# Kernel optimization log

Measured on AMD Instinct MI355X. Metric: run time of the kernel, lower is better.

The kernel has to match this reference:

```python
import jax, jax.numpy as jnp
import numpy as np

B, T, H, C = 32, 2048, 1024, 1024

def setup_inputs() -> dict:
    key = jax.random.key(0)
    k1, k2, k3, k4, k5, k6 = jax.random.split(key, 6)
    decoder_output = jax.random.normal(k1, (B, 1, H), dtype=jnp.float32)
    encoder_outputs = jax.random.normal(k2, (B, T, H), dtype=jnp.float32)
    scale = 1.0 / np.sqrt(H)
    W = jax.random.normal(k3, (H, C), dtype=jnp.float32) * scale
    V = jax.random.normal(k4, (H, C), dtype=jnp.float32) * scale
    b = jax.random.uniform(k5, (C,), dtype=jnp.float32, minval=-0.1, maxval=0.1)
    w = jax.random.normal(k6, (C, 1), dtype=jnp.float32) * (1.0 / np.sqrt(C))
    return {"decoder_output": decoder_output, "encoder_outputs": encoder_outputs,
            "W": W, "V": V, "b": b, "w": w}

def reference(decoder_output, encoder_outputs, W, V, b, w):
    # Additive (Bahdanau) content attention.
    dec_proj = jnp.einsum('bqh,hc->bqc', decoder_output, W)   # [B,1,C]
    enc_proj = jnp.einsum('bth,hc->btc', encoder_outputs, V)  # [B,T,C]
    energy = jnp.tanh(dec_proj + enc_proj + b)                # [B,T,C]
    scores = jnp.einsum('btc,c->bt', energy, w[:, 0])         # [B,T]
    alignment = jax.nn.softmax(scores, axis=-1)               # [B,T]
    context = jnp.einsum('bt,bth->bh', alignment, encoder_outputs)  # [B,H]
    return context
```

## Files before the change

### kernel.cpp

```cpp
#include <hip/hip_runtime.h>
#include <hip/hip_bf16.h>
#include <stdint.h>

#define Bn 32
#define Tn 2048
#define Hn 1024
#define Cn 1024

typedef short short8 __attribute__((ext_vector_type(8)));
typedef float floatx4 __attribute__((ext_vector_type(4)));

__device__ __forceinline__ unsigned int bf16_rne(float f) {
    union { float f; unsigned int u; } v; v.f = f;
    unsigned int u = v.u;
    return (u + 0x7fffu + ((u >> 16) & 1u)) >> 16;
}

__global__ void k_dbias(const float* __restrict__ dec, const float* __restrict__ W,
                        const float* __restrict__ bias, float* __restrict__ dbias) {
    const int b  = blockIdx.x;
    const int c  = blockIdx.y * 256 + threadIdx.x;
    const int h0 = blockIdx.z * 256;
    const float* dv = dec + b * Hn + h0;
    const float* wp = W + (size_t)h0 * Cn + c;
    float acc = 0.f;
#pragma unroll 8
    for (int h = 0; h < 256; ++h)
        acc += dv[h] * wp[(size_t)h * Cn];
    if (blockIdx.z == 0) acc += bias[c];
    atomicAdd(&dbias[b * Cn + c], acc);
}

__global__ void k_vpack(const float* __restrict__ V, uint4* __restrict__ vp) {
    const int bid  = blockIdx.x;
    const int nt   = bid >> 5;
    const int kt   = bid & 31;
    const int lane = threadIdx.x;
    const int c    = nt * 16 + (lane & 15);
    const int k0   = kt * 32 + (lane >> 4) * 8;
    unsigned int h[8];
#pragma unroll
    for (int j = 0; j < 8; ++j)
        h[j] = bf16_rne(V[(size_t)(k0 + j) * Cn + c]);
    uint4 u;
    u.x = h[0] | (h[1] << 16);
    u.y = h[2] | (h[3] << 16);
    u.z = h[4] | (h[5] << 16);
    u.w = h[6] | (h[7] << 16);
    vp[(size_t)bid * 64 + lane] = u;
}

#define BLK_M 64
#define LDA   1032

struct ScoresShared {
    unsigned short A[BLK_M * LDA];
    float scores[BLK_M];
};

__global__ __launch_bounds__(512, 2)
void k_scores(const float* __restrict__ enc, const uint4* __restrict__ vp,
              const float* __restrict__ dbias, const float* __restrict__ wv,
              float* __restrict__ scores_g) {
    __shared__ ScoresShared sh;
    const int wg   = blockIdx.x;
    const int tid  = threadIdx.x;
    const int lane = tid & 63;
    const int wave = tid >> 6;
    const int b    = wg >> 5;
    const int row0 = wg * BLK_M;
    const int lhi  = lane >> 4;
    const int llo  = lane & 15;

    if (tid < BLK_M) sh.scores[tid] = 0.f;

    {
        const float4* ep = (const float4*)(enc + (size_t)row0 * Hn);
#pragma unroll 4
        for (int it = 0; it < 32; ++it) {
            int idx = tid + it * 512;
            int r   = idx >> 8;
            int c4  = idx & 255;
            float4 f = ep[r * 256 + c4];
            uint2 p;
            p.x = bf16_rne(f.x) | (bf16_rne(f.y) << 16);
            p.y = bf16_rne(f.z) | (bf16_rne(f.w) << 16);
            *(uint2*)&sh.A[r * LDA + c4 * 4] = p;
        }
    }
    __syncthreads();

    float score_part[16];
#pragma unroll
    for (int i = 0; i < 16; ++i) score_part[i] = 0.f;

    for (int ni = 0; ni < 2; ++ni) {
        const int colbase = (ni * 8 + wave) * 64;
        const int nt0     = colbase >> 4;

        floatx4 acc[4][4];
#pragma unroll
        for (int i = 0; i < 4; ++i)
#pragma unroll
            for (int j = 0; j < 4; ++j)
                acc[i][j] = (floatx4){0.f, 0.f, 0.f, 0.f};

#pragma unroll 2
        for (int kt = 0; kt < 32; ++kt) {
            short8 afr[4], bfr[4];
#pragma unroll
            for (int rg = 0; rg < 4; ++rg) {
                const unsigned short* ap = &sh.A[(rg * 16 + llo) * LDA + kt * 32 + lhi * 8];
                afr[rg] = *(const short8*)ap;
            }
#pragma unroll
            for (int j = 0; j < 4; ++j) {
                uint4 u = vp[((nt0 + j) * 32 + kt) * 64 + lane];
                bfr[j] = __builtin_bit_cast(short8, u);
            }
#pragma unroll
            for (int rg = 0; rg < 4; ++rg)
#pragma unroll
                for (int j = 0; j < 4; ++j)
                    acc[rg][j] = __builtin_amdgcn_mfma_f32_16x16x32_bf16(
                        afr[rg], bfr[j], acc[rg][j], 0, 0, 0);
        }

#pragma unroll
        for (int j = 0; j < 4; ++j) {
            const int c  = colbase + j * 16 + llo;
            const float db = dbias[b * Cn + c];
            const float wc = wv[c];
#pragma unroll
            for (int rg = 0; rg < 4; ++rg) {
#pragma unroll
                for (int r = 0; r < 4; ++r) {
                    float x = acc[rg][j][r] + db;
                    x = fminf(fmaxf(x, -12.f), 12.f);
                    float e = __expf(2.f * x);
                    float t = 1.f - 2.f / (e + 1.f);
                    score_part[rg * 4 + r] += t * wc;
                }
            }
        }
    }

#pragma unroll
    for (int i = 0; i < 16; ++i) {
        float v = score_part[i];
        v += __shfl_xor(v, 1);
        v += __shfl_xor(v, 2);
        v += __shfl_xor(v, 4);
        v += __shfl_xor(v, 8);
        score_part[i] = v;
    }
    if (llo == 0) {
#pragma unroll
        for (int rg = 0; rg < 4; ++rg)
#pragma unroll
            for (int r = 0; r < 4; ++r)
                atomicAdd(&sh.scores[rg * 16 + lhi * 4 + r], score_part[rg * 4 + r]);
    }
    __syncthreads();
    if (tid < BLK_M) scores_g[row0 + tid] = sh.scores[tid];
}

__global__ void k_softmax(const float* __restrict__ scores, float* __restrict__ align) {
    const int b   = blockIdx.x;
    const int tid = threadIdx.x;
    const float* s = scores + b * Tn;
    float v[8];
    float lmax = -1e30f;
#pragma unroll
    for (int i = 0; i < 8; ++i) { v[i] = s[tid + i * 256]; lmax = fmaxf(lmax, v[i]); }
    for (int off = 1; off < 64; off <<= 1) lmax = fmaxf(lmax, __shfl_xor(lmax, off));
    __shared__ float red[4];
    __shared__ float red2[4];
    if ((tid & 63) == 0) red[tid >> 6] = lmax;
    __syncthreads();
    lmax = fmaxf(fmaxf(red[0], red[1]), fmaxf(red[2], red[3]));
    float lsum = 0.f;
#pragma unroll
    for (int i = 0; i < 8; ++i) { v[i] = __expf(v[i] - lmax); lsum += v[i]; }
    for (int off = 1; off < 64; off <<= 1) lsum += __shfl_xor(lsum, off);
    if ((tid & 63) == 0) red2[tid >> 6] = lsum;
    __syncthreads();
    lsum = red2[0] + red2[1] + red2[2] + red2[3];
    const float inv = 1.f / lsum;
#pragma unroll
    for (int i = 0; i < 8; ++i) align[b * Tn + tid + i * 256] = v[i] * inv;
}

__global__ void k_context(const float* __restrict__ enc, const float* __restrict__ align,
                          float* __restrict__ out) {
    const int b   = blockIdx.x;
    const int tc  = blockIdx.y;
    const int tid = threadIdx.x;
    const float4* ep = (const float4*)(enc + ((size_t)b * Tn + tc * 256) * Hn);
    const float*  al = align + b * Tn + tc * 256;
    float4 acc = {0.f, 0.f, 0.f, 0.f};
    for (int t = 0; t < 256; ++t) {
        const float a = al[t];
        const float4 e = ep[t * 256 + tid];
        acc.x += a * e.x; acc.y += a * e.y; acc.z += a * e.z; acc.w += a * e.w;
    }
    float* op = out + b * Hn + tid * 4;
    atomicAdd(op + 0, acc.x);
    atomicAdd(op + 1, acc.y);
    atomicAdd(op + 2, acc.z);
    atomicAdd(op + 3, acc.w);
}

extern "C" void kernel_launch(void* const* d_in, const int* in_sizes, int n_in,
                              void* d_out, int out_size, void* d_ws, size_t ws_size,
                              hipStream_t stream) {
    const float* dec  = (const float*)d_in[0];
    const float* enc  = (const float*)d_in[1];
    const float* W    = (const float*)d_in[2];
    const float* V    = (const float*)d_in[3];
    const float* bias = (const float*)d_in[4];
    const float* wv   = (const float*)d_in[5];
    float* out = (float*)d_out;

    char* ws = (char*)d_ws;
    float* dbias  = (float*)(ws);
    uint4* vpack  = (uint4*)(ws + 131072);
    float* scores = (float*)(ws + 131072 + 2097152);
    float* align  = (float*)(ws + 131072 + 2097152 + 262144);

    hipMemsetAsync(dbias, 0, 131072, stream);
    hipMemsetAsync(d_out, 0, Bn * Cn * sizeof(float), stream);

    k_dbias  <<<dim3(32, 4, 4), 256, 0, stream>>>(dec, W, bias, dbias);
    k_vpack  <<<2048, 64, 0, stream>>>(V, vpack);
    k_scores <<<1024, 512, 0, stream>>>(enc, vpack, dbias, wv, scores);
    k_softmax<<<32, 256, 0, stream>>>(scores, align);
    k_context<<<dim3(32, 8), 256, 0, stream>>>(enc, align, out);
}
```

Measured before the change: 571.5 us.

## Pipeline encoder tile loads and V fragment prefetch in scores kernel; split context

The scores kernel now loads the encoder tile in four K-chunks and overlaps the global loads and bf16 conversion of each next chunk with MFMA work on the current chunk. It also prefetches the packed V fragments one K-step ahead in registers, and keeps one accumulator set that is zeroed after each column pass. The context kernel uses 64-row slices over a 32x32 grid with unrolling, giving more parallel blocks in exchange for more atomics. Register pressure rises and extra barriers appear in the first column pass.

```diff
diff --git a/kernel.cpp b/kernel.cpp
--- a/kernel.cpp
+++ b/kernel.cpp
@@ -74,61 +74,101 @@
 
     if (tid < BLK_M) sh.scores[tid] = 0.f;
 
-    {
-        const float4* ep = (const float4*)(enc + (size_t)row0 * Hn);
-#pragma unroll 4
-        for (int it = 0; it < 32; ++it) {
-            int idx = tid + it * 512;
-            int r   = idx >> 8;
-            int c4  = idx & 255;
-            float4 f = ep[r * 256 + c4];
-            uint2 p;
-            p.x = bf16_rne(f.x) | (bf16_rne(f.y) << 16);
-            p.y = bf16_rne(f.z) | (bf16_rne(f.w) << 16);
-            *(uint2*)&sh.A[r * LDA + c4 * 4] = p;
+    const float4* ep = (const float4*)(enc + (size_t)row0 * Hn);
+
+    float4 f[8];
+#pragma unroll
+    for (int i = 0; i < 8; ++i) {
+        int idx = tid + i * 512;
+        f[i] = ep[(idx >> 6) * 256 + (idx & 63)];
+    }
+    uint4 bcur[4];
+#pragma unroll
+    for (int j = 0; j < 4; ++j)
+        bcur[j] = vp[((wave * 4 + j) * 32 + 0) * 64 + lane];
+#pragma unroll
+    for (int i = 0; i < 8; ++i) {
+        int idx = tid + i * 512;
+        int r = idx >> 6, c4 = idx & 63;
+        uint2 p;
+        p.x = bf16_rne(f[i].x) | (bf16_rne(f[i].y) << 16);
+        p.y = bf16_rne(f[i].z) | (bf16_rne(f[i].w) << 16);
+        *(uint2*)&sh.A[r * LDA + c4 * 4] = p;
+    }
+    __syncthreads();
+
+    float score_part[16];
+#pragma unroll
+    for (int i = 0; i < 16; ++i) score_part[i] = 0.f;
+
+    floatx4 acc[4][4];
+#pragma unroll
+    for (int i = 0; i < 4; ++i)
+#pragma unroll
+        for (int j = 0; j < 4; ++j)
+            acc[i][j] = (floatx4){0.f, 0.f, 0.f, 0.f};
+
+    for (int ni = 0; ni < 2; ++ni) {
+        for (int ck = 0; ck < 4; ++ck) {
+            if (ni == 0 && ck < 3) {
+#pragma unroll
+                for (int i = 0; i < 8; ++i) {
+                    int idx = tid + i * 512;
+                    f[i] = ep[(idx >> 6) * 256 + (ck + 1) * 64 + (idx & 63)];
+                }
+            }
+
+#pragma unroll
+            for (int k8 = 0; k8 < 8; ++k8) {
+                const int kt = ck * 8 + k8;
+
+                short8 afr[4];
+#pragma unroll
+                for (int rg = 0; rg < 4; ++rg)
+                    afr[rg] = *(const short8*)&sh.A[(rg * 16 + llo) * LDA + kt * 32 + lhi * 8];
+
+                uint4 bn[4];
+                const bool haveNext = !(ni == 1 && kt == 31);
+                if (haveNext) {
+                    const int s1  = ni * 32 + kt + 1;
+                    const int nt1 = ((s1 >> 5) * 8 + wave) * 4;
+                    const int kt1 = s1 & 31;
+#pragma unroll
+                    for (int j = 0; j < 4; ++j)
+                        bn[j] = vp[((nt1 + j) * 32 + kt1) * 64 + lane];
+                }
+
+#pragma unroll
+                for (int rg = 0; rg < 4; ++rg)
+#pragma unroll
+                    for (int j = 0; j < 4; ++j)
+                        acc[rg][j] = __builtin_amdgcn_mfma_f32_16x16x32_bf16(
+                            afr[rg], __builtin_bit_cast(short8, bcur[j]), acc[rg][j], 0, 0, 0);
+
+                if (haveNext) {
+#pragma unroll
+                    for (int j = 0; j < 4; ++j) bcur[j] = bn[j];
+                }
+            }
+
+            if (ni == 0 && ck < 3) {
+#pragma unroll
+                for (int i = 0; i < 8; ++i) {
+                    int idx = tid + i * 512;
+                    int r = idx >> 6, c4 = idx & 63;
+                    uint2 p;
+                    p.x = bf16_rne(f[i].x) | (bf16_rne(f[i].y) << 16);
+                    p.y = bf16_rne(f[i].z) | (bf16_rne(f[i].w) << 16);
+                    *(uint2*)&sh.A[r * LDA + (ck + 1) * 256 + c4 * 4] = p;
+                }
+                __syncthreads();
+            }
         }
-    }
-    __syncthreads();
-
-    float score_part[16];
-#pragma unroll
-    for (int i = 0; i < 16; ++i) score_part[i] = 0.f;
-
-    for (int ni = 0; ni < 2; ++ni) {
+
         const int colbase = (ni * 8 + wave) * 64;
-        const int nt0     = colbase >> 4;
-
-        floatx4 acc[4][4];
-#pragma unroll
-        for (int i = 0; i < 4; ++i)
-#pragma unroll
-            for (int j = 0; j < 4; ++j)
-                acc[i][j] = (floatx4){0.f, 0.f, 0.f, 0.f};
-
-#pragma unroll 2
-        for (int kt = 0; kt < 32; ++kt) {
-            short8 afr[4], bfr[4];
-#pragma unroll
-            for (int rg = 0; rg < 4; ++rg) {
-                const unsigned short* ap = &sh.A[(rg * 16 + llo) * LDA + kt * 32 + lhi * 8];
-                afr[rg] = *(const short8*)ap;
-            }
-#pragma unroll
-            for (int j = 0; j < 4; ++j) {
-                uint4 u = vp[((nt0 + j) * 32 + kt) * 64 + lane];
-                bfr[j] = __builtin_bit_cast(short8, u);
-            }
-#pragma unroll
-            for (int rg = 0; rg < 4; ++rg)
-#pragma unroll
-                for (int j = 0; j < 4; ++j)
-                    acc[rg][j] = __builtin_amdgcn_mfma_f32_16x16x32_bf16(
-                        afr[rg], bfr[j], acc[rg][j], 0, 0, 0);
-        }
-
 #pragma unroll
         for (int j = 0; j < 4; ++j) {
-            const int c  = colbase + j * 16 + llo;
+            const int c   = colbase + j * 16 + llo;
             const float db = dbias[b * Cn + c];
             const float wc = wv[c];
 #pragma unroll
@@ -140,6 +180,7 @@
                     float e = __expf(2.f * x);
                     float t = 1.f - 2.f / (e + 1.f);
                     score_part[rg * 4 + r] += t * wc;
+                    acc[rg][j][r] = 0.f;
                 }
             }
         }
@@ -196,10 +237,11 @@
     const int b   = blockIdx.x;
     const int tc  = blockIdx.y;
     const int tid = threadIdx.x;
-    const float4* ep = (const float4*)(enc + ((size_t)b * Tn + tc * 256) * Hn);
-    const float*  al = align + b * Tn + tc * 256;
+    const float4* ep = (const float4*)(enc + ((size_t)b * Tn + tc * 64) * Hn);
+    const float*  al = align + b * Tn + tc * 64;
     float4 acc = {0.f, 0.f, 0.f, 0.f};
-    for (int t = 0; t < 256; ++t) {
+#pragma unroll 4
+    for (int t = 0; t < 64; ++t) {
         const float a = al[t];
         const float4 e = ep[t * 256 + tid];
         acc.x += a * e.x; acc.y += a * e.y; acc.z += a * e.z; acc.w += a * e.w;
@@ -235,5 +277,5 @@
     k_vpack  <<<2048, 64, 0, stream>>>(V, vpack);
     k_scores <<<1024, 512, 0, stream>>>(enc, vpack, dbias, wv, scores);
     k_softmax<<<32, 256, 0, stream>>>(scores, align);
-    k_context<<<dim3(32, 8), 256, 0, stream>>>(enc, align, out);
-}
+    k_context<<<dim3(32, 32), 256, 0, stream>>>(enc, align, out);
+}
```

Result: slower. 596.1 us (+4.3%).
